# Kernel tuning notes

Measured on AMD Instinct MI355X. Metric: run time of the kernel, lower is better.

## Reference

```python
import jax, jax.numpy as jnp
import numpy as np
import math

H = 512
N2 = 32  # N // 2
L_VAL = 8192
DT_MIN, DT_MAX = 0.001, 0.1


def setup_inputs() -> dict:
    key = jax.random.key(0)
    k1, k2, k3 = jax.random.split(key, 3)
    log_dt = jax.random.uniform(k1, (H,), dtype=jnp.float32) * (
        math.log(DT_MAX) - math.log(DT_MIN)) + math.log(DT_MIN)
    B_real = jax.random.normal(k2, (H, N2), dtype=jnp.float32)
    B_imag = jax.random.normal(k3, (H, N2), dtype=jnp.float32)
    C = jnp.ones((H, N2), dtype=jnp.float32)
    Kc = jnp.ones((H, N2), dtype=jnp.float32)
    A_real = jnp.log(0.5 * jnp.ones((H, N2), dtype=jnp.float32))
    A_imag = jnp.broadcast_to(math.pi * jnp.arange(N2, dtype=jnp.float32), (H, N2))
    return {"log_dt": log_dt, "B_real": B_real, "B_imag": B_imag,
            "C": C, "Kc": Kc, "A_real": A_real, "A_imag": A_imag, "L": L_VAL}


def reference(log_dt, B_real, B_imag, C, Kc, A_real, A_imag, L):
    dt = jnp.exp(log_dt)[:, None]                      # (H, 1)
    A = -jnp.exp(A_real) - 1e-6 + 1j * A_imag          # (H, N2) complex
    denom = 1.0 - dt * A / 2 + 1e-6                    # bilinear denominator
    dtA = (1.0 + dt * A / 2) / denom                   # discretized A (H, N2)
    B = B_real + 1j * B_imag
    dtB = dt * B / denom                               # discretized B (H, N2)
    log_dtA = jnp.log(dtA)                             # complex log
    # Vandermonde in log space: (H, N2, L) complex — the big intermediate.
    V = jnp.exp(log_dtA[:, :, None] * jnp.arange(L, dtype=jnp.float32))
    Cc = C.astype(dtB.dtype) * dtB                     # (H, N2) complex
    K = 2.0 * jnp.einsum('hn,hnl->hl', Cc, V).real     # (H, L)
    return K
```

## Files before the change

### kernel.cpp

```cpp
#include <hip/hip_runtime.h>
#include <math.h>

#define HN   512
#define N2M  32
#define LVAL 8192
#define TPB  512
#define STR  136
#define STRD 68

typedef _Float16 f16x8 __attribute__((ext_vector_type(8)));
typedef __fp16   pk16x2 __attribute__((ext_vector_type(2)));
typedef float    f32x4 __attribute__((ext_vector_type(4)));

__device__ __forceinline__ void split_store_pk(unsigned* dhi, unsigned* dlo,
                                               float x, float y) {
    const pk16x2 hi = __builtin_amdgcn_cvt_pkrtz(x, y);
    const float rx = x - (float)hi.x;
    const float ry = y - (float)hi.y;
    const pk16x2 lo = __builtin_amdgcn_cvt_pkrtz(rx, ry);
    *dhi = __builtin_bit_cast(unsigned, hi);
    *dlo = __builtin_bit_cast(unsigned, lo);
}

__global__ __launch_bounds__(TPB, 4) void s4d_mfma(
    const float* __restrict__ log_dt,
    const float* __restrict__ B_real,
    const float* __restrict__ B_imag,
    const float* __restrict__ Cmat,
    const float* __restrict__ A_real,
    const float* __restrict__ A_imag,
    float* __restrict__ out)
{
    __shared__ __align__(16) _Float16 shU[128 * STR];
    __shared__ __align__(16) _Float16 shW[64 * STR];

    const int h = blockIdx.x;
    const int t = threadIdx.x;
    const int n  = t >> 4;
    const int lg = t & 15;

    const int idx = h * N2M + n;
    const float dt  = expf(log_dt[h]);
    const float Are = -expf(A_real[idx]) - 1e-6f;
    const float Aim = A_imag[idx];
    const float hdt = 0.5f * dt;
    const float dre  = 1.0f - hdt * Are + 1e-6f;
    const float dim_ = -hdt * Aim;
    const float nre = 1.0f + hdt * Are;
    const float nim = hdt * Aim;
    const float inv = 1.0f / (dre * dre + dim_ * dim_);
    const float zr = (nre * dre + nim * dim_) * inv;
    const float zi = (nim * dre - nre * dim_) * inv;
    const float br = B_real[idx], bi = B_imag[idx];
    const float tbr = dt * ((br * dre + bi * dim_) * inv);
    const float tbi = dt * ((bi * dre - br * dim_) * inv);
    const float Cv = Cmat[idx];
    const float c2r = 2.0f * Cv * tbr;
    const float c2i = 2.0f * Cv * tbi;
    const float r2  = zr * zr + zi * zi;
    const float xl2 = 0.5f * log2f(r2);
    const float phi = atan2f(zi, zr) * 0.15915494309189535f;
    const float ph  = __uint_as_float(__float_as_uint(phi) & 0xFFFFE000u);
    const float pl  = phi - ph;
    const float e16  = __builtin_amdgcn_exp2f(16.0f * xl2);
    const float rv16 = __builtin_amdgcn_fractf(
        fmaf(16.0f, pl, __builtin_amdgcn_fractf(16.0f * ph)));
    const float z16r = e16 * __builtin_amdgcn_cosf(rv16);
    const float z16i = e16 * __builtin_amdgcn_sinf(rv16);
    const float e1k  = __builtin_amdgcn_exp2f(1024.0f * xl2);
    const float rv1k = __builtin_amdgcn_fractf(
        fmaf(1024.0f, pl, __builtin_amdgcn_fractf(1024.0f * ph)));
    const float zkr = e1k * __builtin_amdgcn_cosf(rv1k);
    const float zki = e1k * __builtin_amdgcn_sinf(rv1k);

    {
        const float jf  = (float)lg;
        const float e   = __builtin_amdgcn_exp2f(jf * xl2);
        const float rev = __builtin_amdgcn_fractf(
            fmaf(jf, pl, __builtin_amdgcn_fractf(jf * ph)));
        float wr = e * __builtin_amdgcn_cosf(rev);
        float wi = e * __builtin_amdgcn_sinf(rev);
        unsigned* dw = (unsigned*)shW;
#pragma unroll
        for (int s = 0; s < 4; ++s) {
            const int j = lg + 16 * s;
            split_store_pk(dw + j * STRD + n, dw + j * STRD + 32 + n, wr, -wi);
            const float nr = wr * z16r - wi * z16i;
            wi = fmaf(wr, z16i, wi * z16r);
            wr = nr;
        }
    }

    {
        const float l0f = (float)(lg << 6);
        const float e   = __builtin_amdgcn_exp2f(l0f * xl2);
        const float rev = __builtin_amdgcn_fractf(
            fmaf(l0f, pl, __builtin_amdgcn_fractf(l0f * ph)));
        const float cs_ = __builtin_amdgcn_cosf(rev);
        const float sn_ = __builtin_amdgcn_sinf(rev);
        float ur = e * fmaf(c2r, cs_, -(c2i * sn_));
        float ui = e * fmaf(c2r, sn_, c2i * cs_);
        unsigned* du = (unsigned*)shU;
#pragma unroll
        for (int s = 0; s < 8; ++s) {
            const int m = lg + 16 * s;
            split_store_pk(du + m * STRD + n, du + m * STRD + 32 + n, ur, ui);
            const float nr = ur * zkr - ui * zki;
            ui = fmaf(ur, zki, ui * zkr);
            ur = nr;
        }
    }
    __syncthreads();

    const int w = t >> 6, lane = t & 63, g = lane >> 4, r = lane & 15;
    const _Float16* ub = shU + (w * 16 + r) * STR + g * 8;
    const f16x8 B0 = *(const f16x8*)(ub);
    const f16x8 B1 = *(const f16x8*)(ub + 32);
    const f16x8 B2 = *(const f16x8*)(ub + 64);
    const f16x8 B3 = *(const f16x8*)(ub + 96);
    float* outp = out + (size_t)h * LVAL;
#pragma unroll
    for (int jt = 0; jt < 4; ++jt) {
        const _Float16* wa = shW + (jt * 16 + r) * STR + g * 8;
        const f16x8 A0 = *(const f16x8*)(wa);
        const f16x8 A1 = *(const f16x8*)(wa + 32);
        const f16x8 A2 = *(const f16x8*)(wa + 64);
        const f16x8 A3 = *(const f16x8*)(wa + 96);
        f32x4 acc = {0.f, 0.f, 0.f, 0.f};
        acc = __builtin_amdgcn_mfma_f32_16x16x32_f16(A0, B0, acc, 0, 0, 0);
        acc = __builtin_amdgcn_mfma_f32_16x16x32_f16(A1, B1, acc, 0, 0, 0);
        acc = __builtin_amdgcn_mfma_f32_16x16x32_f16(A2, B0, acc, 0, 0, 0);
        acc = __builtin_amdgcn_mfma_f32_16x16x32_f16(A3, B1, acc, 0, 0, 0);
        acc = __builtin_amdgcn_mfma_f32_16x16x32_f16(A0, B2, acc, 0, 0, 0);
        acc = __builtin_amdgcn_mfma_f32_16x16x32_f16(A1, B3, acc, 0, 0, 0);
        float4 v = make_float4(acc[0], acc[1], acc[2], acc[3]);
        *(float4*)(outp + 64 * (16 * w + r) + 16 * jt + 4 * g) = v;
    }
}

extern "C" void kernel_launch(void* const* d_in, const int* in_sizes, int n_in,
                              void* d_out, int out_size, void* d_ws, size_t ws_size,
                              hipStream_t stream)
{
    const float* log_dt = (const float*)d_in[0];
    const float* B_real = (const float*)d_in[1];
    const float* B_imag = (const float*)d_in[2];
    const float* Cmat   = (const float*)d_in[3];
    const float* A_real = (const float*)d_in[5];
    const float* A_imag = (const float*)d_in[6];
    float* out = (float*)d_out;

    s4d_mfma<<<dim3(HN), dim3(TPB), 0, stream>>>(log_dt, B_real, B_imag, Cmat,
                                                 A_real, A_imag, out);
}
```

Baseline: 12.07 us.

## Split each head's sequence across two blocks of 256 threads

The grid becomes (2, H), and each 256-thread block computes half of the L=8192 outputs for one head. Each thread now handles one of 8 lanes per mode instead of 16, so the W factor table is built with stride-8 powers and the U table with stride-512 powers from a per-block offset. The U table in shared memory halves. This is meant to raise the number of blocks for better occupancy and load balance across CUs. The cost is that every block now repeats the per-head discretization and W table setup.

```diff
diff --git a/kernel.cpp b/kernel.cpp
--- a/kernel.cpp
+++ b/kernel.cpp
@@ -4,7 +4,7 @@
 #define HN   512
 #define N2M  32
 #define LVAL 8192
-#define TPB  512
+#define TPB  256
 #define STR  136
 #define STRD 68
 
@@ -31,13 +31,14 @@
     const float* __restrict__ A_imag,
     float* __restrict__ out)
 {
-    __shared__ __align__(16) _Float16 shU[128 * STR];
+    __shared__ __align__(16) _Float16 shU[64 * STR];
     __shared__ __align__(16) _Float16 shW[64 * STR];
 
-    const int h = blockIdx.x;
-    const int t = threadIdx.x;
-    const int n  = t >> 4;
-    const int lg = t & 15;
+    const int h  = blockIdx.y;
+    const int bx = blockIdx.x;
+    const int t  = threadIdx.x;
+    const int n  = t >> 3;
+    const int lg = t & 7;
 
     const int idx = h * N2M + n;
     const float dt  = expf(log_dt[h]);
@@ -62,16 +63,16 @@
     const float phi = atan2f(zi, zr) * 0.15915494309189535f;
     const float ph  = __uint_as_float(__float_as_uint(phi) & 0xFFFFE000u);
     const float pl  = phi - ph;
-    const float e16  = __builtin_amdgcn_exp2f(16.0f * xl2);
-    const float rv16 = __builtin_amdgcn_fractf(
-        fmaf(16.0f, pl, __builtin_amdgcn_fractf(16.0f * ph)));
-    const float z16r = e16 * __builtin_amdgcn_cosf(rv16);
-    const float z16i = e16 * __builtin_amdgcn_sinf(rv16);
-    const float e1k  = __builtin_amdgcn_exp2f(1024.0f * xl2);
-    const float rv1k = __builtin_amdgcn_fractf(
-        fmaf(1024.0f, pl, __builtin_amdgcn_fractf(1024.0f * ph)));
-    const float zkr = e1k * __builtin_amdgcn_cosf(rv1k);
-    const float zki = e1k * __builtin_amdgcn_sinf(rv1k);
+    const float e8  = __builtin_amdgcn_exp2f(8.0f * xl2);
+    const float rv8 = __builtin_amdgcn_fractf(
+        fmaf(8.0f, pl, __builtin_amdgcn_fractf(8.0f * ph)));
+    const float z8r = e8 * __builtin_amdgcn_cosf(rv8);
+    const float z8i = e8 * __builtin_amdgcn_sinf(rv8);
+    const float e5  = __builtin_amdgcn_exp2f(512.0f * xl2);
+    const float rv5 = __builtin_amdgcn_fractf(
+        fmaf(512.0f, pl, __builtin_amdgcn_fractf(512.0f * ph)));
+    const float z5r = e5 * __builtin_amdgcn_cosf(rv5);
+    const float z5i = e5 * __builtin_amdgcn_sinf(rv5);
 
     {
         const float jf  = (float)lg;
@@ -82,17 +83,17 @@
         float wi = e * __builtin_amdgcn_sinf(rev);
         unsigned* dw = (unsigned*)shW;
 #pragma unroll
-        for (int s = 0; s < 4; ++s) {
-            const int j = lg + 16 * s;
+        for (int s = 0; s < 8; ++s) {
+            const int j = lg + 8 * s;
             split_store_pk(dw + j * STRD + n, dw + j * STRD + 32 + n, wr, -wi);
-            const float nr = wr * z16r - wi * z16i;
-            wi = fmaf(wr, z16i, wi * z16r);
+            const float nr = wr * z8r - wi * z8i;
+            wi = fmaf(wr, z8i, wi * z8r);
             wr = nr;
         }
     }
 
     {
-        const float l0f = (float)(lg << 6);
+        const float l0f = (float)((bx << 12) + (lg << 6));
         const float e   = __builtin_amdgcn_exp2f(l0f * xl2);
         const float rev = __builtin_amdgcn_fractf(
             fmaf(l0f, pl, __builtin_amdgcn_fractf(l0f * ph)));
@@ -103,10 +104,10 @@
         unsigned* du = (unsigned*)shU;
 #pragma unroll
         for (int s = 0; s < 8; ++s) {
-            const int m = lg + 16 * s;
+            const int m = lg + 8 * s;
             split_store_pk(du + m * STRD + n, du + m * STRD + 32 + n, ur, ui);
-            const float nr = ur * zkr - ui * zki;
-            ui = fmaf(ur, zki, ui * zkr);
+            const float nr = ur * z5r - ui * z5i;
+            ui = fmaf(ur, z5i, ui * z5r);
             ur = nr;
         }
     }
@@ -118,7 +119,7 @@
     const f16x8 B1 = *(const f16x8*)(ub + 32);
     const f16x8 B2 = *(const f16x8*)(ub + 64);
     const f16x8 B3 = *(const f16x8*)(ub + 96);
-    float* outp = out + (size_t)h * LVAL;
+    float* outp = out + (size_t)h * LVAL + (bx << 12);
 #pragma unroll
     for (int jt = 0; jt < 4; ++jt) {
         const _Float16* wa = shW + (jt * 16 + r) * STR + g * 8;
@@ -150,6 +151,7 @@
     const float* A_imag = (const float*)d_in[6];
     float* out = (float*)d_out;
 
-    s4d_mfma<<<dim3(HN), dim3(TPB), 0, stream>>>(log_dt, B_real, B_imag, Cmat,
-                                                 A_real, A_imag, out);
+    dim3 grid(2, HN);
+    s4d_mfma<<<grid, dim3(TPB), 0, stream>>>(log_dt, B_real, B_imag, Cmat,
+                                             A_real, A_imag, out);
 }
```

Measured after the change: 11.76 us. 2.5% less time.
